# Kernel tuning notes

Hardware: AMD Instinct MI355X
Metric: run time of the kernel (lower is better)

## Reference

```python
import jax, jax.numpy as jnp
import numpy as np

# 24 unique dyadic offsets (powers of 2 and 3*2^k), max < N
UNIQUE_OFFSETS = np.array([0, 1, 2, 3, 4, 6, 8, 12, 16, 24, 32, 48, 64, 96, 128,
                           192, 256, 384, 512, 768, 1024, 1536, 2048, 3072], dtype=np.int32)
B, N, D, H = 1, 4096, 1024, 16
HD = D // H


def setup_inputs() -> dict:
    key = jax.random.key(0)
    ks = jax.random.split(key, 8)
    s = D ** -0.5
    return {
        "x": jax.random.normal(ks[0], (B, N, D), jnp.float32),
        "Wqkv": jax.random.normal(ks[1], (D, 3 * D), jnp.float32) * s,
        "bqkv": jnp.zeros((3 * D,), jnp.float32),
        "Wout": jax.random.normal(ks[2], (D, D), jnp.float32) * s,
        "bout": jnp.zeros((D,), jnp.float32),
        "Wgate": jax.random.normal(ks[3], (D, D), jnp.float32) * s,
        "bgate": jnp.full((D,), 2.0, jnp.float32),  # nn.init.constant_(gate_proj.bias, 2.0)
        "pos_bias": jax.random.normal(ks[4], (len(UNIQUE_OFFSETS), H), jnp.float32) * 0.1,
    }


def reference(x, Wqkv, bqkv, Wout, bout, Wgate, bgate, pos_bias):
    b, n, d = x.shape
    scale = HD ** -0.5
    qkv = x @ Wqkv + bqkv                       # [B,N,3D]
    q, k, v = jnp.split(qkv, 3, axis=-1)
    def heads(t):
        return t.reshape(b, n, H, HD).transpose(0, 2, 1, 3)  # [B,H,N,HD]
    q, k, v = heads(q), heads(k), heads(v)

    deltas = jnp.asarray(UNIQUE_OFFSETS)        # [O]
    idx = jnp.arange(n)[:, None] - deltas[None, :]   # [N,O] source position t-delta
    valid = (idx >= 0).astype(x.dtype)[:, :, None]   # [N,O,1]; covers delta>=N too
    idxc = jnp.clip(idx, 0, n - 1)

    k_g = k[:, :, idxc, :] * valid              # [B,H,N,O,HD] gathered, zero-padded
    v_g = v[:, :, idxc, :] * valid

    # score_{t,i} = q_t . k_{t-delta_i} * scale + pos_bias[i, head]
    scores = jnp.einsum('bhnd,bhnod->bhno', q, k_g) * scale + pos_bias.T[None, :, None, :]
    attn = jax.nn.softmax(scores, axis=-1)      # softmax over 24 taps
    out = jnp.einsum('bhno,bhnod->bhnd', attn, v_g)

    out_flat = out.transpose(0, 2, 1, 3).reshape(b, n, d)
    gate = jax.nn.sigmoid(x @ Wgate + bgate)
    return (out_flat * gate) @ Wout + bout      # dropout is identity in eval
```

## Files before the change

### kernel.cpp

```cpp
#include <hip/hip_runtime.h>
#include <hip/hip_bf16.h>

#define NN 4096
#define DD 1024
#define HH 16
#define HDD 64
#define NO 24
#define QG_N 4096

typedef short bf16x8 __attribute__((ext_vector_type(8)));
typedef float f32x4 __attribute__((ext_vector_type(4)));
typedef unsigned short ushort;

__device__ __forceinline__ ushort f2bf(float f) {
    unsigned u = __float_as_uint(f);
    return (ushort)((u + 0x7FFFu + ((u >> 16) & 1u)) >> 16);
}
__device__ __forceinline__ float bf2f(ushort u) {
    return __uint_as_float(((unsigned)u) << 16);
}

__device__ __forceinline__ void gload16(const void* g, void* l) {
    __builtin_amdgcn_global_load_lds((const __attribute__((address_space(1))) void*)g,
                                     (__attribute__((address_space(3))) void*)l, 16, 0, 0);
}

__device__ __forceinline__ int tap_delta(int j) {
    return j < 2 ? j : (2 + (j & 1)) << ((j >> 1) - 1);
}

__global__ __launch_bounds__(256) void f2b_kernel(const float* __restrict__ in,
                                                  ushort* __restrict__ out, int n4) {
    int i = blockIdx.x * 256 + threadIdx.x;
    if (i < n4) {
        float4 v = ((const float4*)in)[i];
        ushort4 o;
        o.x = f2bf(v.x); o.y = f2bf(v.y); o.z = f2bf(v.z); o.w = f2bf(v.w);
        ((ushort4*)out)[i] = o;
    }
}

__global__ __launch_bounds__(256) void transpose_f2b(const float* __restrict__ in,
                                                     ushort* __restrict__ out,
                                                     int R, int C) {
    __shared__ float tile[32][33];
    const int c0 = blockIdx.x * 32, r0 = blockIdx.y * 32;
    const int tx = threadIdx.x & 31, ty = threadIdx.x >> 5;
#pragma unroll
    for (int i = 0; i < 32; i += 8)
        tile[ty + i][tx] = in[(size_t)(r0 + ty + i) * C + c0 + tx];
    __syncthreads();
#pragma unroll
    for (int i = 0; i < 32; i += 8)
        out[(size_t)(c0 + ty + i) * R + r0 + tx] = f2bf(tile[tx][ty + i]);
}

template <int OP>
__global__ __launch_bounds__(256) void mfma_gemm(const ushort* __restrict__ A,
                                                 const ushort* __restrict__ BT,
                                                 const float* __restrict__ bias0,
                                                 const float* __restrict__ bias1,
                                                 int sigStart,
                                                 void* __restrict__ Cout,
                                                 int M, int N, int K) {
    __shared__ ushort sA[2][128 * 32];
    __shared__ ushort sB[2][128 * 32];

    const int tid = threadIdx.x;
    const int lane = tid & 63;
    const int w = tid >> 6;
    const int wr = w >> 1, wc = w & 1;
    const int m0 = blockIdx.y * 128, n0 = blockIdx.x * 128;

    const int row0 = tid >> 2, slot = tid & 3;
    const int row1 = row0 + 64;
    const int sw0 = slot ^ ((row0 >> 1) & 3);
    const int sw1 = slot ^ ((row1 >> 1) & 3);
    const int dst0 = (tid & ~63) * 8;
    const int dst1 = (256 + (tid & ~63)) * 8;

    const size_t aOff0 = (size_t)(m0 + row0) * K + sw0 * 8;
    const size_t aOff1 = (size_t)(m0 + row1) * K + sw1 * 8;
    const size_t bOff0 = (size_t)(n0 + row0) * K + sw0 * 8;
    const size_t bOff1 = (size_t)(n0 + row1) * K + sw1 * 8;

    const int ks = lane >> 4;
    int aRd[4], bRd[4];
#pragma unroll
    for (int m = 0; m < 4; ++m) {
        int r = wr * 64 + m * 16 + (lane & 15);
        aRd[m] = r * 64 + ((ks ^ ((r >> 1) & 3)) << 4);
    }
#pragma unroll
    for (int n = 0; n < 4; ++n) {
        int r = wc * 64 + n * 16 + (lane & 15);
        bRd[n] = r * 64 + ((ks ^ ((r >> 1) & 3)) << 4);
    }

    f32x4 acc[4][4];
#pragma unroll
    for (int m = 0; m < 4; ++m)
#pragma unroll
        for (int n = 0; n < 4; ++n) acc[m][n] = (f32x4){0.f, 0.f, 0.f, 0.f};

#define STAGE(buf, k0)                                              \
    do {                                                            \
        gload16(A + aOff0 + (k0), &sA[buf][dst0]);                  \
        gload16(A + aOff1 + (k0), &sA[buf][dst1]);                  \
        gload16(BT + bOff0 + (k0), &sB[buf][dst0]);                 \
        gload16(BT + bOff1 + (k0), &sB[buf][dst1]);                 \
    } while (0)

    const int NS = K >> 5;
    STAGE(0, 0);
    for (int s = 0; s < NS; ++s) {
        const int cur = s & 1;
        __syncthreads();
        if (s + 1 < NS) STAGE(cur ^ 1, (s + 1) * 32);
        const char* pa = (const char*)sA[cur];
        const char* pb = (const char*)sB[cur];
        bf16x8 af[4], bfr[4];
#pragma unroll
        for (int m = 0; m < 4; ++m) af[m] = *(const bf16x8*)(pa + aRd[m]);
#pragma unroll
        for (int n = 0; n < 4; ++n) bfr[n] = *(const bf16x8*)(pb + bRd[n]);
#pragma unroll
        for (int m = 0; m < 4; ++m)
#pragma unroll
            for (int n = 0; n < 4; ++n)
                acc[m][n] = __builtin_amdgcn_mfma_f32_16x16x32_bf16(af[m], bfr[n],
                                                                    acc[m][n], 0, 0, 0);
    }
#undef STAGE

    const int fr = lane & 15, fq = lane >> 4;
#pragma unroll
    for (int m = 0; m < 4; ++m) {
        const int rbase = m0 + wr * 64 + m * 16 + fq * 4;
#pragma unroll
        for (int n = 0; n < 4; ++n) {
            const int col = n0 + wc * 64 + n * 16 + fr;
            const bool sig = (col >= sigStart);
            const float bv = sig ? bias1[col - sigStart] : bias0[col];
#pragma unroll
            for (int j = 0; j < 4; ++j) {
                float v = acc[m][n][j] + bv;
                if (sig) v = 1.f / (1.f + expf(-v));
                if (OP == 0) {
                    ((float*)Cout)[(size_t)(rbase + j) * N + col] = v;
                } else {
                    ((ushort*)Cout)[(size_t)(rbase + j) * N + col] = f2bf(v);
                }
            }
        }
    }
}

__global__ __launch_bounds__(256) void attn_kernel(const ushort* __restrict__ qkvg,
                                                   const float* __restrict__ pos_bias,
                                                   ushort* __restrict__ outp) {
    const int bid = (blockIdx.x & 7) * 2048 + (blockIdx.x >> 3);
    const int w = threadIdx.x >> 6;
    const int lane = threadIdx.x & 63;
    const int g = lane >> 3;
    const int e = lane & 7;
    const int h = bid >> 10;
    const int t = (bid & 1023) * 4 + w;

    const int d0 = h * HDD + e * 8;

    bf16x8 q8 = *(const bf16x8*)(qkvg + (size_t)t * QG_N + d0);
    float qf[8];
#pragma unroll
    for (int i = 0; i < 8; ++i) qf[i] = bf2f((ushort)q8[i]);

    float sc[3];
    float pv_p[3];
    int rowz[3];
    bool valid[3];
#pragma unroll
    for (int r = 0; r < 3; ++r) {
        const int j = 8 * r + g;
        const int dlt = tap_delta(j);
        valid[r] = (t >= dlt);
        rowz[r] = valid[r] ? (t - dlt) : 0;
        bf16x8 k8 = *(const bf16x8*)(qkvg + (size_t)rowz[r] * QG_N + DD + d0);
        float dot = 0.f;
#pragma unroll
        for (int i = 0; i < 8; ++i) dot = fmaf(qf[i], bf2f((ushort)k8[i]), dot);
        dot += __shfl_xor(dot, 1);
        dot += __shfl_xor(dot, 2);
        dot += __shfl_xor(dot, 4);
        const float pb = pos_bias[j * HH + h];
        sc[r] = valid[r] ? fmaf(dot, 0.125f, pb) : pb;
    }

    float mx = fmaxf(fmaxf(sc[0], sc[1]), sc[2]);
    mx = fmaxf(mx, __shfl_xor(mx, 8));
    mx = fmaxf(mx, __shfl_xor(mx, 16));
    mx = fmaxf(mx, __shfl_xor(mx, 32));
    float ex[3];
#pragma unroll
    for (int r = 0; r < 3; ++r) ex[r] = __expf(sc[r] - mx);
    float den = ex[0] + ex[1] + ex[2];
    den += __shfl_xor(den, 8);
    den += __shfl_xor(den, 16);
    den += __shfl_xor(den, 32);
    const float inv = 1.f / den;
#pragma unroll
    for (int r = 0; r < 3; ++r) pv_p[r] = valid[r] ? ex[r] * inv : 0.f;

    float o[8];
#pragma unroll
    for (int i = 0; i < 8; ++i) o[i] = 0.f;
#pragma unroll
    for (int r = 0; r < 3; ++r) {
        bf16x8 v8 = *(const bf16x8*)(qkvg + (size_t)rowz[r] * QG_N + 2 * DD + d0);
#pragma unroll
        for (int i = 0; i < 8; ++i) o[i] = fmaf(pv_p[r], bf2f((ushort)v8[i]), o[i]);
    }
#pragma unroll
    for (int i = 0; i < 8; ++i) {
        o[i] += __shfl_xor(o[i], 8);
        o[i] += __shfl_xor(o[i], 16);
        o[i] += __shfl_xor(o[i], 32);
    }

    if (g == 0) {
        bf16x8 g8 = *(const bf16x8*)(qkvg + (size_t)t * QG_N + 3 * DD + d0);
        bf16x8 o8;
#pragma unroll
        for (int i = 0; i < 8; ++i)
            o8[i] = (short)f2bf(o[i] * bf2f((ushort)g8[i]));
        *(bf16x8*)(outp + (size_t)t * DD + d0) = o8;
    }
}

extern "C" void kernel_launch(void* const* d_in, const int* in_sizes, int n_in,
                              void* d_out, int out_size, void* d_ws, size_t ws_size,
                              hipStream_t stream) {
    const float* x = (const float*)d_in[0];
    const float* Wqkv = (const float*)d_in[1];
    const float* bqkv = (const float*)d_in[2];
    const float* Wout = (const float*)d_in[3];
    const float* bout = (const float*)d_in[4];
    const float* Wgate = (const float*)d_in[5];
    const float* bgate = (const float*)d_in[6];
    const float* pos_bias = (const float*)d_in[7];
    float* out = (float*)d_out;

    char* ws = (char*)d_ws;
    ushort* xb = (ushort*)ws;
    ushort* WcatT = (ushort*)(ws + ((size_t)8 << 20));
    ushort* WoutT = (ushort*)(ws + ((size_t)16 << 20));
    ushort* qkvg = (ushort*)(ws + ((size_t)18 << 20));
    ushort* gated = (ushort*)(ws + ((size_t)50 << 20));

    f2b_kernel<<<(NN * DD / 4 + 255) / 256, 256, 0, stream>>>(x, xb, NN * DD / 4);
    transpose_f2b<<<dim3(3 * DD / 32, DD / 32), 256, 0, stream>>>(Wqkv, WcatT, DD, 3 * DD);
    transpose_f2b<<<dim3(DD / 32, DD / 32), 256, 0, stream>>>(
        Wgate, WcatT + (size_t)3 * DD * DD, DD, DD);
    transpose_f2b<<<dim3(DD / 32, DD / 32), 256, 0, stream>>>(Wout, WoutT, DD, DD);

    mfma_gemm<1><<<dim3(QG_N / 128, NN / 128), 256, 0, stream>>>(
        xb, WcatT, bqkv, bgate, 3 * DD, qkvg, NN, QG_N, DD);
    attn_kernel<<<16384, 256, 0, stream>>>(qkvg, pos_bias, gated);
    mfma_gemm<0><<<dim3(DD / 128, NN / 128), 256, 0, stream>>>(
        gated, WoutT, bout, bout, 1 << 30, out, NN, DD, DD);
}
```

Before: 207.0 us.

## Add 256x256-tile 8-wave GEMM with split-phase LDS pipeline for QKV+gate projection

Replaces the 128x128 GEMM used for the fused QKV+gate projection with a new 512-thread kernel that computes 256x256 tiles. It uses 128 KB of dynamic LDS with double buffering, 64-wide K steps, XOR-swizzled direct global-to-LDS loads, and four interleaved load/MFMA phases with s_setprio around the MFMA blocks. A grid swizzle is added for L2 locality. The goal is more data reuse per LDS byte and better overlap of memory with MFMA work, at the cost of much higher register pressure, a single block per CU, and only 256 blocks, which may underfill the GPU. The output GEMM is simplified to drop the unused sigmoid path.

New measurement: 195.4 us. -5.6%, faster.

```diff
diff --git a/kernel.cpp b/kernel.cpp
--- a/kernel.cpp
+++ b/kernel.cpp
@@ -24,6 +24,13 @@
     __builtin_amdgcn_global_load_lds((const __attribute__((address_space(1))) void*)g,
                                      (__attribute__((address_space(3))) void*)l, 16, 0, 0);
 }
+
+#define BAR()                                  \
+    do {                                       \
+        asm volatile("" ::: "memory");         \
+        __builtin_amdgcn_s_barrier();          \
+        asm volatile("" ::: "memory");         \
+    } while (0)
 
 __device__ __forceinline__ int tap_delta(int j) {
     return j < 2 ? j : (2 + (j & 1)) << ((j >> 1) - 1);
@@ -55,12 +62,154 @@
         out[(size_t)(c0 + ty + i) * R + r0 + tx] = f2bf(tile[tx][ty + i]);
 }
 
+__global__ __launch_bounds__(512) void mfma_gemm256(const ushort* __restrict__ A,
+                                                    const ushort* __restrict__ BT,
+                                                    const float* __restrict__ bias0,
+                                                    const float* __restrict__ bias1,
+                                                    int sigStart,
+                                                    ushort* __restrict__ Cout,
+                                                    int M, int N, int K) {
+    extern __shared__ char lds[];
+
+    const int tid = threadIdx.x;
+    const int lane = tid & 63;
+    const int wid = tid >> 6;
+    const int wr = wid >> 2;
+    const int wc = wid & 3;
+
+    const int id = blockIdx.y * gridDim.x + blockIdx.x;
+    const int swz = (id & 7) * 32 + (id >> 3);
+    const int m0 = (swz >> 4) * 256, n0 = (swz & 15) * 256;
+
+    const int sw = (tid & 7) ^ ((tid >> 3) & 7);
+    const int srow = tid >> 3;
+    const size_t aBase = (size_t)(m0 + srow) * K + sw * 8;
+    const size_t bBase = (size_t)(n0 + srow) * K + sw * 8;
+    const int ldst = (tid & ~63) * 16;
+
+#define ISSUE_A(buf, i, k0) \
+    gload16(A + aBase + (size_t)(i) * 64 * K + (k0), lds + (buf) * 65536 + (i) * 8192 + ldst)
+#define ISSUE_B(buf, i, k0) \
+    gload16(BT + bBase + (size_t)(i) * 64 * K + (k0), lds + (buf) * 65536 + 32768 + (i) * 8192 + ldst)
+
+    const int lr = lane & 15;
+    const int l47 = lane >> 4;
+    const int r7 = lr & 7;
+
+#define A_OFF(mf, ks) \
+    (((mf) * 32 + wr * 16 + lr) * 128 + ((((ks) * 4 + l47) ^ r7) << 4))
+#define B_OFF(nf, ks) \
+    (32768 + ((nf) * 64 + wc * 16 + lr) * 128 + ((((ks) * 4 + l47) ^ r7) << 4))
+
+    f32x4 acc[8][4];
+#pragma unroll
+    for (int m = 0; m < 8; ++m)
+#pragma unroll
+        for (int n = 0; n < 4; ++n) acc[m][n] = (f32x4){0.f, 0.f, 0.f, 0.f};
+
+    bf16x8 ar[4][2], br[2][2];
+
+#define LOAD_A_HALF(buf, h)                                                     \
+    do {                                                                        \
+        const char* p = lds + (buf) * 65536;                                    \
+        _Pragma("unroll") for (int m2 = 0; m2 < 4; ++m2)                        \
+            _Pragma("unroll") for (int ks = 0; ks < 2; ++ks)                    \
+                ar[m2][ks] = *(const bf16x8*)(p + A_OFF((h) * 4 + m2, ks));     \
+    } while (0)
+#define LOAD_B_HALF(buf, h)                                                     \
+    do {                                                                        \
+        const char* p = lds + (buf) * 65536;                                    \
+        _Pragma("unroll") for (int n2 = 0; n2 < 2; ++n2)                        \
+            _Pragma("unroll") for (int ks = 0; ks < 2; ++ks)                    \
+                br[n2][ks] = *(const bf16x8*)(p + B_OFF((h) * 2 + n2, ks));     \
+    } while (0)
+#define MFMA_QUAD(ah, bh)                                                       \
+    do {                                                                        \
+        __builtin_amdgcn_s_setprio(1);                                          \
+        _Pragma("unroll") for (int m2 = 0; m2 < 4; ++m2)                        \
+            _Pragma("unroll") for (int n2 = 0; n2 < 2; ++n2)                    \
+                _Pragma("unroll") for (int ks = 0; ks < 2; ++ks)                \
+                    acc[(ah) * 4 + m2][(bh) * 2 + n2] =                         \
+                        __builtin_amdgcn_mfma_f32_16x16x32_bf16(                \
+                            ar[m2][ks], br[n2][ks],                             \
+                            acc[(ah) * 4 + m2][(bh) * 2 + n2], 0, 0, 0);        \
+        __builtin_amdgcn_s_setprio(0);                                          \
+    } while (0)
+
+    ISSUE_A(0, 0, 0); ISSUE_A(0, 1, 0);
+    ISSUE_B(0, 0, 0); ISSUE_B(0, 1, 0);
+    ISSUE_A(0, 2, 0); ISSUE_A(0, 3, 0);
+    ISSUE_B(0, 2, 0); ISSUE_B(0, 3, 0);
+
+    const int NT = K >> 6;
+    for (int t = 0; t < NT; ++t) {
+        const int buf = t & 1;
+        const int nxt = buf ^ 1;
+        const int nk = (t + 1) * 64;
+        const bool pf = (t + 1 < NT);
+
+        asm volatile("s_waitcnt vmcnt(4)" ::: "memory");
+        BAR();
+        LOAD_A_HALF(buf, 0);
+        LOAD_B_HALF(buf, 0);
+        if (pf) { ISSUE_A(nxt, 0, nk); ISSUE_A(nxt, 1, nk); }
+        BAR();
+        MFMA_QUAD(0, 0);
+
+        if (pf) {
+            asm volatile("s_waitcnt vmcnt(2)" ::: "memory");
+        } else {
+            asm volatile("s_waitcnt vmcnt(0)" ::: "memory");
+        }
+        BAR();
+        LOAD_B_HALF(buf, 1);
+        if (pf) { ISSUE_B(nxt, 0, nk); ISSUE_B(nxt, 1, nk); }
+        BAR();
+        MFMA_QUAD(0, 1);
+
+        BAR();
+        LOAD_A_HALF(buf, 1);
+        if (pf) { ISSUE_A(nxt, 2, nk); ISSUE_A(nxt, 3, nk); }
+        BAR();
+        MFMA_QUAD(1, 1);
+
+        BAR();
+        LOAD_B_HALF(buf, 0);
+        if (pf) { ISSUE_B(nxt, 2, nk); ISSUE_B(nxt, 3, nk); }
+        BAR();
+        MFMA_QUAD(1, 0);
+    }
+
+    const int fr = lane & 15, fq = lane >> 4;
+#pragma unroll
+    for (int mf = 0; mf < 8; ++mf) {
+        const int row = m0 + mf * 32 + wr * 16 + fq * 4;
+#pragma unroll
+        for (int nf = 0; nf < 4; ++nf) {
+            const int col = n0 + nf * 64 + wc * 16 + fr;
+            const bool sig = (col >= sigStart);
+            const float bv = sig ? bias1[col - sigStart] : bias0[col];
+#pragma unroll
+            for (int j = 0; j < 4; ++j) {
+                float v = acc[mf][nf][j] + bv;
+                if (sig) v = 1.f / (1.f + expf(-v));
+                Cout[(size_t)(row + j) * N + col] = f2bf(v);
+            }
+        }
+    }
+#undef ISSUE_A
+#undef ISSUE_B
+#undef A_OFF
+#undef B_OFF
+#undef LOAD_A_HALF
+#undef LOAD_B_HALF
+#undef MFMA_QUAD
+}
+
 template <int OP>
 __global__ __launch_bounds__(256) void mfma_gemm(const ushort* __restrict__ A,
                                                  const ushort* __restrict__ BT,
                                                  const float* __restrict__ bias0,
-                                                 const float* __restrict__ bias1,
-                                                 int sigStart,
                                                  void* __restrict__ Cout,
                                                  int M, int N, int K) {
     __shared__ ushort sA[2][128 * 32];
@@ -140,17 +289,10 @@
 #pragma unroll
         for (int n = 0; n < 4; ++n) {
             const int col = n0 + wc * 64 + n * 16 + fr;
-            const bool sig = (col >= sigStart);
-            const float bv = sig ? bias1[col - sigStart] : bias0[col];
+            const float bv = bias0[col];
 #pragma unroll
             for (int j = 0; j < 4; ++j) {
-                float v = acc[m][n][j] + bv;
-                if (sig) v = 1.f / (1.f + expf(-v));
-                if (OP == 0) {
-                    ((float*)Cout)[(size_t)(rbase + j) * N + col] = v;
-                } else {
-                    ((ushort*)Cout)[(size_t)(rbase + j) * N + col] = f2bf(v);
-                }
+                ((float*)Cout)[(size_t)(rbase + j) * N + col] = acc[m][n][j] + bv;
             }
         }
     }
@@ -262,9 +404,11 @@
         Wgate, WcatT + (size_t)3 * DD * DD, DD, DD);
     transpose_f2b<<<dim3(DD / 32, DD / 32), 256, 0, stream>>>(Wout, WoutT, DD, DD);
 
-    mfma_gemm<1><<<dim3(QG_N / 128, NN / 128), 256, 0, stream>>>(
+    hipFuncSetAttribute(reinterpret_cast<const void*>(mfma_gemm256),
+                        hipFuncAttributeMaxDynamicSharedMemorySize, 131072);
+    mfma_gemm256<<<dim3(16, 16), 512, 131072, stream>>>(
         xb, WcatT, bqkv, bgate, 3 * DD, qkvg, NN, QG_N, DD);
     attn_kernel<<<16384, 256, 0, stream>>>(qkvg, pos_bias, gated);
     mfma_gemm<0><<<dim3(DD / 128, NN / 128), 256, 0, stream>>>(
-        gated, WoutT, bout, bout, 1 << 30, out, NN, DD, DD);
-}
+        gated, WoutT, bout, out, NN, DD, DD);
+}
```
